# Kernel optimization log

Measured on AMD Instinct MI355X. Metric: run time of the kernel, lower is better.

## Reference

```python
import jax, jax.numpy as jnp
import numpy as np

HEAD_SIZE = 8
MODEL_SIZE = 512
K_SIZE = 64
V_SIZE = 64
B, L = 4, 2048


def setup_inputs() -> dict:
    key = jax.random.key(0)
    ks = jax.random.split(key, 12)
    s = 0.02
    inp = {
        "q": jax.random.normal(ks[0], (B, L, MODEL_SIZE), jnp.float32),
        "k": jax.random.normal(ks[1], (B, L, MODEL_SIZE), jnp.float32),
        "v": jax.random.normal(ks[2], (B, L, MODEL_SIZE), jnp.float32),
        "attn_mask": jax.random.randint(ks[3], (B, L, L), 0, 2).astype(jnp.bool_),
        "Wq": jax.random.normal(ks[4], (K_SIZE, MODEL_SIZE), jnp.float32) * s,
        "bq": jnp.zeros((K_SIZE,), jnp.float32),
        "Wk": jax.random.normal(ks[5], (K_SIZE, MODEL_SIZE), jnp.float32) * s,
        "bk": jnp.zeros((K_SIZE,), jnp.float32),
        "Wv": jax.random.normal(ks[6], (V_SIZE, MODEL_SIZE), jnp.float32) * s,
        "bv": jnp.zeros((V_SIZE,), jnp.float32),
        "Wp": jax.random.normal(ks[7], (MODEL_SIZE, HEAD_SIZE * V_SIZE), jnp.float32) * s,
        "bp": jnp.zeros((MODEL_SIZE,), jnp.float32),
    }
    return inp


def reference(q, k, v, attn_mask, Wq, bq, Wk, bk, Wv, bv, Wp, bp):
    # Original module applies the same linear_q/k/v to head-repeated tensors,
    # so every head is identical; compute once and tile (exactly equal math).
    temperature = jnp.asarray(MODEL_SIZE, q.dtype) ** 0.5  # note: sqrt(model_size), not sqrt(k_size)
    qp = jnp.einsum('bld,kd->blk', q, Wq) + bq  # (B, Lq, k_size)
    kp = jnp.einsum('bld,kd->blk', k, Wk) + bk  # (B, Lk, k_size)
    vp = jnp.einsum('bld,kd->blk', v, Wv) + bv  # (B, Lk, v_size)
    attn = jnp.einsum('bqd,bkd->bqk', qp, kp) / temperature  # (B, Lq, Lk)
    attn = jnp.where(attn_mask, -jnp.inf, attn)
    attn = jax.nn.softmax(attn, axis=-1)  # dropout is identity at eval
    out = jnp.einsum('bqk,bkd->bqd', attn, vp)  # (B, Lq, v_size)
    out = jnp.tile(out, (1, 1, HEAD_SIZE))  # concat of identical per-head outputs
    out = jnp.einsum('blh,mh->blm', out, Wp) + bp  # (B, Lq, model_size)
    return out
```

## Files before the change

kernel.cpp:

```cpp
#include <hip/hip_runtime.h>

#define B_ 4
#define L_ 2048
#define MD_ 512
#define KV_ 64
#define NKT_ (L_ / 64)
#define KSPLIT 8
#define NT_ (NKT_ / KSPLIT)

typedef unsigned short u16;
typedef unsigned char u8;
typedef unsigned int u32;
typedef unsigned long long u64;
typedef __attribute__((ext_vector_type(8))) short bf16x8;
typedef __attribute__((ext_vector_type(4))) float f32x4;
typedef __attribute__((ext_vector_type(4))) u32 u32x4;
typedef __attribute__((ext_vector_type(4))) u16 u16x4;

#define INV_T 0.044194173824159216f

static __device__ __forceinline__ u16 f2bf(float x) {
  u32 u = __float_as_uint(x);
  return (u16)((u + 0x7FFFu + ((u >> 16) & 1u)) >> 16);
}
static __device__ __forceinline__ f32x4 zero4() {
  f32x4 z = {0.f, 0.f, 0.f, 0.f};
  return z;
}
static __device__ __forceinline__ f32x4 mfma16(bf16x8 a, bf16x8 b, f32x4 c) {
  return __builtin_amdgcn_mfma_f32_16x16x32_bf16(a, b, c, 0, 0, 0);
}

__global__ __launch_bounds__(256) void mha_prep(
    const float* __restrict__ Wq, const float* __restrict__ Wk,
    const float* __restrict__ Wv, const float* __restrict__ bq,
    const float* __restrict__ bk, const float* __restrict__ bv,
    const float* __restrict__ Wp, u16* __restrict__ WtT,
    float* __restrict__ bqkv, u16* __restrict__ WpT) {
  int t = blockIdx.x * 256 + threadIdx.x;
  if (t < 3 * 64 * 512) {
    int p = t >> 15, c = (t >> 9) & 63, d = t & 511;
    const float* W = (p == 0) ? Wq : ((p == 1) ? Wk : Wv);
    WtT[(p * 64 + c) * 520 + d] = f2bf(W[c * 512 + d]);
  } else if (t < 3 * 64 * 512 + 512 * 64) {
    int i = t - 3 * 64 * 512;
    int m = i >> 6, d = i & 63;
    float s = 0.f;
#pragma unroll
    for (int h = 0; h < 8; h++) s += Wp[m * 512 + h * 64 + d];
    WpT[m * 72 + d] = f2bf(s);
  } else if (t < 3 * 64 * 512 + 512 * 64 + 192) {
    int j = t - (3 * 64 * 512 + 512 * 64);
    int p = j >> 6;
    const float* bb = (p == 0) ? bq : ((p == 1) ? bk : bv);
    bqkv[j] = bb[j & 63];
  }
}

__global__ __launch_bounds__(256) void mha_mask(const int* __restrict__ mask,
                                                u64* __restrict__ pkm) {
  const int tid = threadIdx.x;
  const int l = tid & 63;
  const size_t wid = (blockIdx.x * 256 + tid) >> 6;
  const size_t NW = 1024 * 4;
  const size_t TOT = (size_t)B_ * L_ * L_;
  for (size_t base = wid * 256; base < TOT; base += NW * 256) {
    u32x4 m = *(const u32x4*)(mask + base + l * 4);
    u64 bal[4];
#pragma unroll
    for (int j = 0; j < 4; j++) bal[j] = __ballot(m[j] != 0);
    if (l < 4) {
      u64 pk = 0;
#pragma unroll
      for (int j = 0; j < 4; j++)
        pk |= ((bal[j] >> (l * 16)) & 0xFFFFull) << (16 * j);
      size_t R = base >> 11;
      int kt0 = (int)((base & 2047) >> 6);
      pkm[R * 32 + kt0 + l] = pk;
    }
  }
}

__global__ __launch_bounds__(256) void mha_proj(
    const float* __restrict__ q, const float* __restrict__ k,
    const float* __restrict__ v, const u16* __restrict__ WtT,
    const float* __restrict__ bqkv, u16* __restrict__ qp,
    u16* __restrict__ kp, u16* __restrict__ vpt) {
  __shared__ __align__(16) u16 X[3][32][520];
  __shared__ __align__(16) u16 Xv[32][72];
  const int tid = threadIdx.x;
  const int r0 = blockIdx.x * 32;
#pragma unroll 4
  for (int i = 0; i < 48; i++) {
    int e = tid + i * 256;
    int p = e >> 12, r = (e >> 7) & 31, dq = (e & 127) << 2;
    const float* src = (p == 0) ? q : ((p == 1) ? k : v);
    f32x4 xv = *(const f32x4*)(src + (size_t)(r0 + r) * 512 + dq);
    u16x4 w4 = {f2bf(xv[0]), f2bf(xv[1]), f2bf(xv[2]), f2bf(xv[3])};
    *(u16x4*)&X[p][r][dq] = w4;
  }
  __syncthreads();
  const int w = tid >> 6, l = tid & 63, g = l >> 4, li = l & 15;
  const int mt = w & 1, half = w >> 1;
  f32x4 acc[6];
#pragma unroll
  for (int i = 0; i < 6; i++) acc[i] = zero4();

  if (half == 0) {
#pragma unroll 4
    for (int ks = 0; ks < 16; ks++) {
      const int ko = g * 8 + ks * 32;
      bf16x8 a0 = *(const bf16x8*)&X[0][mt * 16 + li][ko];
      bf16x8 a1 = *(const bf16x8*)&X[1][mt * 16 + li][ko];
      acc[0] = mfma16(a0, *(const bf16x8*)(WtT + (0 * 64 + 0 + li) * 520 + ko), acc[0]);
      acc[1] = mfma16(a0, *(const bf16x8*)(WtT + (0 * 64 + 16 + li) * 520 + ko), acc[1]);
      acc[2] = mfma16(a0, *(const bf16x8*)(WtT + (0 * 64 + 32 + li) * 520 + ko), acc[2]);
      acc[3] = mfma16(a0, *(const bf16x8*)(WtT + (0 * 64 + 48 + li) * 520 + ko), acc[3]);
      acc[4] = mfma16(a1, *(const bf16x8*)(WtT + (1 * 64 + 0 + li) * 520 + ko), acc[4]);
      acc[5] = mfma16(a1, *(const bf16x8*)(WtT + (1 * 64 + 16 + li) * 520 + ko), acc[5]);
    }
  } else {
#pragma unroll 4
    for (int ks = 0; ks < 16; ks++) {
      const int ko = g * 8 + ks * 32;
      bf16x8 a1 = *(const bf16x8*)&X[1][mt * 16 + li][ko];
      bf16x8 a2 = *(const bf16x8*)&X[2][mt * 16 + li][ko];
      acc[0] = mfma16(a1, *(const bf16x8*)(WtT + (1 * 64 + 32 + li) * 520 + ko), acc[0]);
      acc[1] = mfma16(a1, *(const bf16x8*)(WtT + (1 * 64 + 48 + li) * 520 + ko), acc[1]);
      acc[2] = mfma16(a2, *(const bf16x8*)(WtT + (2 * 64 + 0 + li) * 520 + ko), acc[2]);
      acc[3] = mfma16(a2, *(const bf16x8*)(WtT + (2 * 64 + 16 + li) * 520 + ko), acc[3]);
      acc[4] = mfma16(a2, *(const bf16x8*)(WtT + (2 * 64 + 32 + li) * 520 + ko), acc[4]);
      acc[5] = mfma16(a2, *(const bf16x8*)(WtT + (2 * 64 + 48 + li) * 520 + ko), acc[5]);
    }
  }
#pragma unroll
  for (int i = 0; i < 6; i++) {
    int nt = half * 6 + i;
    int p = nt >> 2, c4 = nt & 3;
    float bias = bqkv[nt * 16 + li];
#pragma unroll
    for (int j = 0; j < 4; j++) {
      int row = r0 + mt * 16 + g * 4 + j;
      u16 val = f2bf(acc[i][j] + bias);
      if (p == 0)
        qp[(size_t)row * 64 + c4 * 16 + li] = val;
      else if (p == 1)
        kp[(size_t)row * 64 + c4 * 16 + li] = val;
      else
        Xv[mt * 16 + g * 4 + j][c4 * 16 + li] = val;
    }
  }
  __syncthreads();
  {
    int d = tid >> 2, ch = tid & 3;
    size_t bb_ = (size_t)(r0 >> 11), kk = (size_t)(r0 & 2047);
    u16 tmp[8];
#pragma unroll
    for (int r = 0; r < 8; r++) tmp[r] = Xv[ch * 8 + r][d];
    *(bf16x8*)(vpt + (bb_ * 64 + d) * 2048 + kk + ch * 8) = *(bf16x8*)tmp;
  }
}

__global__ __launch_bounds__(256, 2) void mha_attn(
    const u16* __restrict__ qp, const u16* __restrict__ kp,
    const u16* __restrict__ vpt, const u64* __restrict__ pkm,
    u16* __restrict__ po, float* __restrict__ pl) {
  __shared__ __align__(16) char Klds[32768];
  __shared__ __align__(16) char Vlds[32768];
  __shared__ __align__(16) u16 Plds[4][16][72];
  const int tid = threadIdx.x;
  const int w = tid >> 6, l = tid & 63, g = l >> 4, li = l & 15;
  const int b = blockIdx.y;
  const int q0 = blockIdx.x * 64;
  const int s = blockIdx.z;
  const size_t brow = (size_t)b * L_;
  const int k0 = s * 256;

#pragma unroll
  for (int i = 0; i < 8; i++) {
    int e = i * 256 + tid;
    int r = e >> 3, c = (e & 7) * 16;
    u32x4 v = *(const u32x4*)(kp + (brow + k0 + r) * 64 + (e & 7) * 8);
    *(u32x4*)(Klds + r * 128 + (c ^ ((r & 7) << 4))) = v;
  }
#pragma unroll
  for (int i = 0; i < 8; i++) {
    int e = i * 256 + tid;
    int d = e >> 5, c = (e & 31) * 16;
    u32x4 v = *(const u32x4*)(vpt + ((size_t)b * 64 + d) * 2048 + k0 +
                              (e & 31) * 8);
    *(u32x4*)(Vlds + d * 512 + (c ^ ((d & 7) << 4))) = v;
  }

  bf16x8 qf0 = *(const bf16x8*)(qp + (brow + q0 + w * 16 + li) * 64 + g * 8);
  bf16x8 qf1 =
      *(const bf16x8*)(qp + (brow + q0 + w * 16 + li) * 64 + g * 8 + 32);
  const u64* prow = pkm + (brow + q0 + w * 16 + li) * 32 + s * NT_;
  u64 pk0 = prow[0], pk1 = prow[1], pk2 = prow[2], pk3 = prow[3];

  f32x4 o[4];
#pragma unroll
  for (int i = 0; i < 4; i++) o[i] = zero4();
  float rsl = 0.f;

  const int cA = (g * 16) ^ ((li & 7) << 4);
  const int cB = (g * 16 + 64) ^ ((li & 7) << 4);
  const int vx = (li & 7) << 4;

  __syncthreads();

#pragma unroll
  for (int kt = 0; kt < NT_; kt++) {
    const u64 pk = (kt == 0) ? pk0 : ((kt == 1) ? pk1 : ((kt == 2) ? pk2 : pk3));
    f32x4 sacc[4];
#pragma unroll
    for (int nt = 0; nt < 4; nt++) {
      const int kr = kt * 64 + nt * 16 + li;
      bf16x8 kf0 = *(const bf16x8*)(Klds + kr * 128 + cA);
      bf16x8 kf1 = *(const bf16x8*)(Klds + kr * 128 + cB);
      sacc[nt] = mfma16(kf0, qf0, zero4());
      sacc[nt] = mfma16(kf1, qf1, sacc[nt]);
    }
#pragma unroll
    for (int nt = 0; nt < 4; nt++) {
      float pv[4];
#pragma unroll
      for (int r = 0; r < 4; r++) {
        float ex = __expf(sacc[nt][r] * INV_T);
        pv[r] = ((pk >> (r * 16 + nt * 4 + g)) & 1) ? 0.f : ex;
        rsl += pv[r];
      }
      u16x4 pkw = {f2bf(pv[0]), f2bf(pv[1]), f2bf(pv[2]), f2bf(pv[3])};
      *(u16x4*)&Plds[w][li][nt * 16 + 4 * g] = pkw;
    }
#pragma unroll
    for (int ks = 0; ks < 2; ks++) {
      bf16x8 pa = *(const bf16x8*)&Plds[w][li][ks * 32 + g * 8];
      const int vcol = (kt * 128 + ks * 64 + g * 16) ^ vx;
#pragma unroll
      for (int dt = 0; dt < 4; dt++) {
        bf16x8 vb = *(const bf16x8*)(Vlds + (dt * 16 + li) * 512 + vcol);
        o[dt] = mfma16(pa, vb, o[dt]);
      }
    }
  }
  rsl += __shfl_xor(rsl, 16);
  rsl += __shfl_xor(rsl, 32);
#pragma unroll
  for (int j = 0; j < 4; j++) {
    size_t r = brow + q0 + w * 16 + g * 4 + j;
    size_t base = (r * KSPLIT + s) * 64;
#pragma unroll
    for (int dt = 0; dt < 4; dt++) po[base + dt * 16 + li] = f2bf(o[dt][j]);
  }
  if (l < 16) pl[(brow + q0 + w * 16 + l) * KSPLIT + s] = rsl;
}

__global__ __launch_bounds__(256) void mha_comb(const u16* __restrict__ po,
                                                const float* __restrict__ pl,
                                                u16* __restrict__ aout) {
  int id = blockIdx.x * 256 + threadIdx.x;
  int r = id >> 6, d = id & 63;
  float L = 0.f, acc = 0.f;
#pragma unroll
  for (int i = 0; i < KSPLIT; i++) {
    L += pl[r * KSPLIT + i];
    u16 u = po[((size_t)(r * KSPLIT + i)) * 64 + d];
    acc += __uint_as_float((u32)u << 16);
  }
  aout[(size_t)r * 64 + d] = f2bf(acc / L);
}

__global__ __launch_bounds__(128) void mha_fin(const u16* __restrict__ aout,
                                               const u16* __restrict__ WpT,
                                               const float* __restrict__ bp,
                                               float* __restrict__ out) {
  const int tid = threadIdx.x;
  const int w = tid >> 6, l = tid & 63, g = l >> 4, li = l & 15;
  const size_t r0 = (size_t)blockIdx.x * 32;
  const u16* ar = aout + (r0 + w * 16 + li) * 64;
  bf16x8 a0 = *(const bf16x8*)(ar + g * 8);
  bf16x8 a1 = *(const bf16x8*)(ar + g * 8 + 32);
#pragma unroll 4
  for (int nt = 0; nt < 32; nt++) {
    bf16x8 b0 = *(const bf16x8*)(WpT + (nt * 16 + li) * 72 + g * 8);
    bf16x8 b1 = *(const bf16x8*)(WpT + (nt * 16 + li) * 72 + g * 8 + 32);
    f32x4 acc = zero4();
    acc = mfma16(a0, b0, acc);
    acc = mfma16(a1, b1, acc);
    float bias = bp[nt * 16 + li];
#pragma unroll
    for (int j = 0; j < 4; j++)
      out[(r0 + w * 16 + g * 4 + j) * 512 + nt * 16 + li] = acc[j] + bias;
  }
}

extern "C" void kernel_launch(void* const* d_in, const int* in_sizes, int n_in,
                              void* d_out, int out_size, void* d_ws,
                              size_t ws_size, hipStream_t stream) {
  const float* q = (const float*)d_in[0];
  const float* k = (const float*)d_in[1];
  const float* v = (const float*)d_in[2];
  const int* mask = (const int*)d_in[3];
  const float* Wq = (const float*)d_in[4];
  const float* bq = (const float*)d_in[5];
  const float* Wk = (const float*)d_in[6];
  const float* bk = (const float*)d_in[7];
  const float* Wv = (const float*)d_in[8];
  const float* bv = (const float*)d_in[9];
  const float* Wp = (const float*)d_in[10];
  const float* bp = (const float*)d_in[11];

  char* ws = (char*)d_ws;
  u16* qp = (u16*)(ws + 0);
  u16* kp = (u16*)(ws + 1048576);
  u16* vpt = (u16*)(ws + 2097152);
  u16* aout = (u16*)(ws + 3145728);
  u16* WtT = (u16*)(ws + 4194304);
  float* bqkv = (float*)(ws + 4393984);
  u16* WpT = (u16*)(ws + 4394752);
  u16* po = (u16*)(ws + 4468736);
  float* pl = (float*)(ws + 12857344);
  u64* pkm = (u64*)(ws + 13119488);

  mha_prep<<<dim3(513), dim3(256), 0, stream>>>(Wq, Wk, Wv, bq, bk, bv, Wp,
                                                WtT, bqkv, WpT);
  mha_mask<<<dim3(1024), dim3(256), 0, stream>>>(mask, pkm);
  mha_proj<<<dim3(256), dim3(256), 0, stream>>>(q, k, v, WtT, bqkv, qp, kp,
                                                vpt);
  mha_attn<<<dim3(32, 4, KSPLIT), dim3(256), 0, stream>>>(qp, kp, vpt, pkm,
                                                          po, pl);
  mha_comb<<<dim3(2048), dim3(256), 0, stream>>>(po, pl, aout);
  mha_fin<<<dim3(256), dim3(128), 0, stream>>>(aout, WpT, bp, (float*)d_out);
}
```

Before: 65.29 us.

## Fuse mask packing into attention, fuse split combine into output projection

Drops the separate mask-packing kernel: each attention block reads its own raw int mask tile, turns it into bitmasks with ballots into shared memory, and interleaves those loads with the K/V staging. The key split goes from 8 to 16, so each block holds 128 keys, uses half the LDS, and is allowed 4 blocks per CU. The combine kernel is folded into the final projection kernel, which sums the partials in shared memory before the MFMA. This removes two launches and the round trips through global memory for the packed mask and the combined output. In exchange, the partial-output traffic doubles with 16 splits.

```diff
diff --git a/kernel.cpp b/kernel.cpp
--- a/kernel.cpp
+++ b/kernel.cpp
@@ -5,8 +5,8 @@
 #define MD_ 512
 #define KV_ 64
 #define NKT_ (L_ / 64)
-#define KSPLIT 8
-#define NT_ (NKT_ / KSPLIT)
+#define KSPLIT 16
+#define NT_ 2
 
 typedef unsigned short u16;
 typedef unsigned char u8;
@@ -22,6 +22,9 @@
 static __device__ __forceinline__ u16 f2bf(float x) {
   u32 u = __float_as_uint(x);
   return (u16)((u + 0x7FFFu + ((u >> 16) & 1u)) >> 16);
+}
+static __device__ __forceinline__ float bf2f(u16 u) {
+  return __uint_as_float((u32)u << 16);
 }
 static __device__ __forceinline__ f32x4 zero4() {
   f32x4 z = {0.f, 0.f, 0.f, 0.f};
@@ -57,30 +60,6 @@
   }
 }
 
-__global__ __launch_bounds__(256) void mha_mask(const int* __restrict__ mask,
-                                                u64* __restrict__ pkm) {
-  const int tid = threadIdx.x;
-  const int l = tid & 63;
-  const size_t wid = (blockIdx.x * 256 + tid) >> 6;
-  const size_t NW = 1024 * 4;
-  const size_t TOT = (size_t)B_ * L_ * L_;
-  for (size_t base = wid * 256; base < TOT; base += NW * 256) {
-    u32x4 m = *(const u32x4*)(mask + base + l * 4);
-    u64 bal[4];
-#pragma unroll
-    for (int j = 0; j < 4; j++) bal[j] = __ballot(m[j] != 0);
-    if (l < 4) {
-      u64 pk = 0;
-#pragma unroll
-      for (int j = 0; j < 4; j++)
-        pk |= ((bal[j] >> (l * 16)) & 0xFFFFull) << (16 * j);
-      size_t R = base >> 11;
-      int kt0 = (int)((base & 2047) >> 6);
-      pkm[R * 32 + kt0 + l] = pk;
-    }
-  }
-}
-
 __global__ __launch_bounds__(256) void mha_proj(
     const float* __restrict__ q, const float* __restrict__ k,
     const float* __restrict__ v, const u16* __restrict__ WtT,
@@ -161,42 +140,84 @@
   }
 }
 
-__global__ __launch_bounds__(256, 2) void mha_attn(
+__global__ __launch_bounds__(256, 4) void mha_attn(
     const u16* __restrict__ qp, const u16* __restrict__ kp,
-    const u16* __restrict__ vpt, const u64* __restrict__ pkm,
+    const u16* __restrict__ vpt, const int* __restrict__ mask,
     u16* __restrict__ po, float* __restrict__ pl) {
-  __shared__ __align__(16) char Klds[32768];
-  __shared__ __align__(16) char Vlds[32768];
+  __shared__ __align__(16) char Klds[16384];
+  __shared__ __align__(16) char Vlds[16384];
   __shared__ __align__(16) u16 Plds[4][16][72];
+  __shared__ __align__(8) u64 Mb[64][2];
   const int tid = threadIdx.x;
   const int w = tid >> 6, l = tid & 63, g = l >> 4, li = l & 15;
   const int b = blockIdx.y;
   const int q0 = blockIdx.x * 64;
   const int s = blockIdx.z;
   const size_t brow = (size_t)b * L_;
-  const int k0 = s * 256;
-
-#pragma unroll
-  for (int i = 0; i < 8; i++) {
+  const int k0 = s * 128;
+
+  const int par = l >> 5, lc = l & 31;
+  const int sh = ((l >> 1) & 1) * 32 + (l & 1) * 16;
+
+  u32x4 mreg[4];
+#pragma unroll
+  for (int c = 0; c < 4; c++) {
+    int rr = (w * 8 + c) * 2 + par;
+    mreg[c] = *(const u32x4*)(mask + (brow + q0 + rr) * (size_t)L_ + k0 + lc * 4);
+  }
+  u32x4 kst[4];
+#pragma unroll
+  for (int i = 0; i < 4; i++) {
     int e = i * 256 + tid;
-    int r = e >> 3, c = (e & 7) * 16;
-    u32x4 v = *(const u32x4*)(kp + (brow + k0 + r) * 64 + (e & 7) * 8);
-    *(u32x4*)(Klds + r * 128 + (c ^ ((r & 7) << 4))) = v;
-  }
-#pragma unroll
-  for (int i = 0; i < 8; i++) {
-    int e = i * 256 + tid;
-    int d = e >> 5, c = (e & 31) * 16;
-    u32x4 v = *(const u32x4*)(vpt + ((size_t)b * 64 + d) * 2048 + k0 +
-                              (e & 31) * 8);
-    *(u32x4*)(Vlds + d * 512 + (c ^ ((d & 7) << 4))) = v;
-  }
-
+    kst[i] = *(const u32x4*)(kp + (brow + k0 + (e >> 3)) * 64 + (e & 7) * 8);
+  }
   bf16x8 qf0 = *(const bf16x8*)(qp + (brow + q0 + w * 16 + li) * 64 + g * 8);
   bf16x8 qf1 =
       *(const bf16x8*)(qp + (brow + q0 + w * 16 + li) * 64 + g * 8 + 32);
-  const u64* prow = pkm + (brow + q0 + w * 16 + li) * 32 + s * NT_;
-  u64 pk0 = prow[0], pk1 = prow[1], pk2 = prow[2], pk3 = prow[3];
+#pragma unroll
+  for (int i = 0; i < 4; i++) {
+    int e = i * 256 + tid;
+    int r = e >> 3, c = (e & 7) * 16;
+    *(u32x4*)(Klds + r * 128 + (c ^ ((r & 7) << 4))) = kst[i];
+  }
+#pragma unroll
+  for (int c = 0; c < 4; c++) {
+    u64 bal[4];
+#pragma unroll
+    for (int j = 0; j < 4; j++) bal[j] = __ballot(mreg[c][j] != 0);
+    u64 pk = 0;
+#pragma unroll
+    for (int j = 0; j < 4; j++) pk |= ((bal[j] >> sh) & 0xFFFFull) << (16 * j);
+    if (l < 4) Mb[(w * 8 + c) * 2 + (l >> 1)][l & 1] = pk;
+  }
+#pragma unroll
+  for (int c = 0; c < 4; c++) {
+    int rr = (w * 8 + 4 + c) * 2 + par;
+    mreg[c] = *(const u32x4*)(mask + (brow + q0 + rr) * (size_t)L_ + k0 + lc * 4);
+  }
+  u32x4 vst[4];
+#pragma unroll
+  for (int i = 0; i < 4; i++) {
+    int e = i * 256 + tid;
+    vst[i] = *(const u32x4*)(vpt + ((size_t)b * 64 + (e >> 4)) * 2048 + k0 +
+                             (e & 15) * 8);
+  }
+#pragma unroll
+  for (int i = 0; i < 4; i++) {
+    int e = i * 256 + tid;
+    int d = e >> 4, c = (e & 15) * 16;
+    *(u32x4*)(Vlds + d * 256 + (c ^ ((d & 7) << 4))) = vst[i];
+  }
+#pragma unroll
+  for (int c = 0; c < 4; c++) {
+    u64 bal[4];
+#pragma unroll
+    for (int j = 0; j < 4; j++) bal[j] = __ballot(mreg[c][j] != 0);
+    u64 pk = 0;
+#pragma unroll
+    for (int j = 0; j < 4; j++) pk |= ((bal[j] >> sh) & 0xFFFFull) << (16 * j);
+    if (l < 4) Mb[(w * 8 + 4 + c) * 2 + (l >> 1)][l & 1] = pk;
+  }
 
   f32x4 o[4];
 #pragma unroll
@@ -211,7 +232,7 @@
 
 #pragma unroll
   for (int kt = 0; kt < NT_; kt++) {
-    const u64 pk = (kt == 0) ? pk0 : ((kt == 1) ? pk1 : ((kt == 2) ? pk2 : pk3));
+    const u64 pk = Mb[w * 16 + li][kt];
     f32x4 sacc[4];
 #pragma unroll
     for (int nt = 0; nt < 4; nt++) {
@@ -239,7 +260,7 @@
       const int vcol = (kt * 128 + ks * 64 + g * 16) ^ vx;
 #pragma unroll
       for (int dt = 0; dt < 4; dt++) {
-        bf16x8 vb = *(const bf16x8*)(Vlds + (dt * 16 + li) * 512 + vcol);
+        bf16x8 vb = *(const bf16x8*)(Vlds + (dt * 16 + li) * 256 + vcol);
         o[dt] = mfma16(pa, vb, o[dt]);
       }
     }
@@ -256,31 +277,42 @@
   if (l < 16) pl[(brow + q0 + w * 16 + l) * KSPLIT + s] = rsl;
 }
 
-__global__ __launch_bounds__(256) void mha_comb(const u16* __restrict__ po,
-                                                const float* __restrict__ pl,
-                                                u16* __restrict__ aout) {
-  int id = blockIdx.x * 256 + threadIdx.x;
-  int r = id >> 6, d = id & 63;
-  float L = 0.f, acc = 0.f;
-#pragma unroll
-  for (int i = 0; i < KSPLIT; i++) {
-    L += pl[r * KSPLIT + i];
-    u16 u = po[((size_t)(r * KSPLIT + i)) * 64 + d];
-    acc += __uint_as_float((u32)u << 16);
-  }
-  aout[(size_t)r * 64 + d] = f2bf(acc / L);
-}
-
-__global__ __launch_bounds__(128) void mha_fin(const u16* __restrict__ aout,
+__global__ __launch_bounds__(128) void mha_fin(const u16* __restrict__ po,
+                                               const float* __restrict__ pl,
                                                const u16* __restrict__ WpT,
                                                const float* __restrict__ bp,
                                                float* __restrict__ out) {
+  __shared__ __align__(16) u16 A[32][72];
   const int tid = threadIdx.x;
+  const size_t r0 = (size_t)blockIdx.x * 32;
+  {
+    const int rr = tid >> 2, dc = tid & 3;
+    float accd[16];
+#pragma unroll
+    for (int j = 0; j < 16; j++) accd[j] = 0.f;
+    float Lsum = 0.f;
+#pragma unroll 4
+    for (int i = 0; i < KSPLIT; i++) {
+      const u16* p = po + ((r0 + rr) * KSPLIT + i) * 64 + dc * 16;
+      u32x4 lo = *(const u32x4*)p;
+      u32x4 hi = *(const u32x4*)(p + 8);
+#pragma unroll
+      for (int j = 0; j < 4; j++) {
+        accd[2 * j + 0] += bf2f((u16)(lo[j] & 0xFFFF));
+        accd[2 * j + 1] += bf2f((u16)(lo[j] >> 16));
+        accd[8 + 2 * j + 0] += bf2f((u16)(hi[j] & 0xFFFF));
+        accd[8 + 2 * j + 1] += bf2f((u16)(hi[j] >> 16));
+      }
+      Lsum += pl[(r0 + rr) * KSPLIT + i];
+    }
+    float inv = 1.f / Lsum;
+#pragma unroll
+    for (int j = 0; j < 16; j++) A[rr][dc * 16 + j] = f2bf(accd[j] * inv);
+  }
+  __syncthreads();
   const int w = tid >> 6, l = tid & 63, g = l >> 4, li = l & 15;
-  const size_t r0 = (size_t)blockIdx.x * 32;
-  const u16* ar = aout + (r0 + w * 16 + li) * 64;
-  bf16x8 a0 = *(const bf16x8*)(ar + g * 8);
-  bf16x8 a1 = *(const bf16x8*)(ar + g * 8 + 32);
+  bf16x8 a0 = *(const bf16x8*)&A[w * 16 + li][g * 8];
+  bf16x8 a1 = *(const bf16x8*)&A[w * 16 + li][g * 8 + 32];
 #pragma unroll 4
   for (int nt = 0; nt < 32; nt++) {
     bf16x8 b0 = *(const bf16x8*)(WpT + (nt * 16 + li) * 72 + g * 8);
@@ -315,21 +347,18 @@
   u16* qp = (u16*)(ws + 0);
   u16* kp = (u16*)(ws + 1048576);
   u16* vpt = (u16*)(ws + 2097152);
-  u16* aout = (u16*)(ws + 3145728);
   u16* WtT = (u16*)(ws + 4194304);
   float* bqkv = (float*)(ws + 4393984);
   u16* WpT = (u16*)(ws + 4394752);
   u16* po = (u16*)(ws + 4468736);
-  float* pl = (float*)(ws + 12857344);
-  u64* pkm = (u64*)(ws + 13119488);
+  float* pl = (float*)(ws + 21245952);
 
   mha_prep<<<dim3(513), dim3(256), 0, stream>>>(Wq, Wk, Wv, bq, bk, bv, Wp,
                                                 WtT, bqkv, WpT);
-  mha_mask<<<dim3(1024), dim3(256), 0, stream>>>(mask, pkm);
   mha_proj<<<dim3(256), dim3(256), 0, stream>>>(q, k, v, WtT, bqkv, qp, kp,
                                                 vpt);
-  mha_attn<<<dim3(32, 4, KSPLIT), dim3(256), 0, stream>>>(qp, kp, vpt, pkm,
+  mha_attn<<<dim3(32, 4, KSPLIT), dim3(256), 0, stream>>>(qp, kp, vpt, mask,
                                                           po, pl);
-  mha_comb<<<dim3(2048), dim3(256), 0, stream>>>(po, pl, aout);
-  mha_fin<<<dim3(256), dim3(128), 0, stream>>>(aout, WpT, bp, (float*)d_out);
-}
+  mha_fin<<<dim3(256), dim3(128), 0, stream>>>(po, pl, WpT, bp,
+                                               (float*)d_out);
+}
```

Result: faster. 59.94 us (-8.2%).
